# Performance work log

Hardware: AMD Instinct MI355X
Metric: run time of the kernel (lower is better)

## Reference

```python
import jax, jax.numpy as jnp
import numpy as np
from functools import partial

B, D, H, T = 1024, 512, 1024, 64  # batch, latent dim, MLP hidden, time points


def setup_inputs() -> dict:
    key = jax.random.key(0)
    k0, k1, k2, k3, k4 = jax.random.split(key, 5)
    z0 = jax.random.normal(k0, (B, D), dtype=jnp.float32)
    # strictly increasing time grid, modest dt for a stable tanh-MLP vector field
    t = jnp.arange(T, dtype=jnp.float32) * 0.02
    # 2-layer tanh MLP ode_func: dz/dt = tanh(z @ W1 + b1) @ W2 + b2
    W1 = jax.random.normal(k1, (D, H), dtype=jnp.float32) * (1.0 / np.sqrt(D))
    b1 = jnp.zeros((H,), dtype=jnp.float32)
    W2 = jax.random.normal(k2, (H, D), dtype=jnp.float32) * (1.0 / np.sqrt(H))
    b2 = jnp.zeros((D,), dtype=jnp.float32)
    return {"z0": z0, "t": t, "W1": W1, "b1": b1, "W2": W2, "b2": b2}


def _ode_func(z, W1, b1, W2, b2):
    # autonomous latent vector field: [B, D] -> [B, D]
    return jnp.tanh(z @ W1 + b1) @ W2 + b2


def reference(z0, t, W1, b1, W2, b2):
    """odeint(ode_func, z0, t, method='rk4'): one classical RK4 step per interval.
    Returns trajectory [T, B, D] with traj[0] == z0 (torchdiffeq convention)."""
    f = partial(_ode_func, W1=W1, b1=b1, W2=W2, b2=b2)
    dts = t[1:] - t[:-1]  # [T-1]

    def step(z, dt):
        k1 = f(z)
        k2 = f(z + 0.5 * dt * k1)
        k3 = f(z + 0.5 * dt * k2)
        k4 = f(z + dt * k3)
        z_new = z + (dt / 6.0) * (k1 + 2.0 * k2 + 2.0 * k3 + k4)
        return z_new, z_new

    _, traj = jax.lax.scan(step, z0, dts)  # [T-1, B, D]
    return jnp.concatenate([z0[None], traj], axis=0)  # [T, B, D]
```

## Files before the change

kernel.cpp:

```cpp
#include <hip/hip_runtime.h>
#include <hip/hip_bf16.h>

#define BATCH 1024
#define DLAT  512
#define HHID  1024
#define TPTS  64
#define BD    (BATCH * DLAT)

#define NBLK 256
#define NTHR 512
#define RGN  16


typedef __attribute__((ext_vector_type(8))) short short8;
typedef __attribute__((ext_vector_type(4))) float f32x4;

__device__ __forceinline__ short f2bf(float x) {
    __hip_bfloat16 h = __float2bfloat16(x);
    return __builtin_bit_cast(short, h);
}
__device__ __forceinline__ float fast_tanh(float x) {
    x = fminf(9.f, fmaxf(-9.f, x));
    const float e = __expf(2.f * x);
    return (e - 1.f) / (e + 1.f);
}

__device__ __forceinline__ void rg_barrier(int* bar, int cidx, int target, int tid)
{
    __syncthreads();
    if (tid == 0) {
        atomicAdd(&bar[cidx], 1);
        while (__hip_atomic_load(&bar[cidx], __ATOMIC_RELAXED,
                                 __HIP_MEMORY_SCOPE_AGENT) < target) {
            __builtin_amdgcn_s_sleep(2);
        }
    }
    __syncthreads();
    asm volatile("buffer_inv\n\ts_waitcnt vmcnt(0)" ::: "memory");
}

__global__ __launch_bounds__(NTHR) void ode_coop(
    const float* __restrict__ z0, const float* __restrict__ t,
    const float* __restrict__ W1, const float* __restrict__ b1,
    const float* __restrict__ W2, const float* __restrict__ b2,
    short* __restrict__ zf, short* __restrict__ Hf,
    int* __restrict__ bar, int* __restrict__ xcnt,
    float* __restrict__ traj)
{
    __shared__ __align__(16) short W1L[4 * 16 * 64 * 8];
    __shared__ __align__(16) short W2L[2 * 32 * 64 * 8];
    __shared__ float b1L[64];
    __shared__ float b2L[32];
    __shared__ int slotS;

    const int tid  = threadIdx.x;
    const int lane = tid & 63;
    const int w    = tid >> 6;
    const int q    = lane >> 4;
    const int cl   = lane & 15;

    unsigned int xcc;
    asm("s_getreg_b32 %0, hwreg(HW_REG_XCC_ID)" : "=s"(xcc));
    xcc &= 7u;
    if (tid == 0) slotS = atomicAdd(&xcnt[xcc], 1);
    __syncthreads();
    const int slot = slotS & 31;
    const int rg   = (int)xcc * 2 + (slot >> 4);
    const int cg   = slot & 15;
    const int cidx = rg * 32;

    for (int i = tid; i < 4 * 16 * 64; i += NTHR) {
        const int ct = i >> 10, kt = (i >> 6) & 15, l = i & 63;
        const int k0 = kt * 32 + (l >> 4) * 8;
        const int n  = cg * 64 + ct * 16 + (l & 15);
        short8 v;
#pragma unroll
        for (int j = 0; j < 8; ++j) v[j] = f2bf(W1[(size_t)(k0 + j) * HHID + n]);
        *(short8*)&W1L[i * 8] = v;
    }
    for (int i = tid; i < 2 * 32 * 64; i += NTHR) {
        const int ct = i >> 11, kt = (i >> 6) & 31, l = i & 63;
        const int k0 = kt * 32 + (l >> 4) * 8;
        const int n  = cg * 32 + ct * 16 + (l & 15);
        short8 v;
#pragma unroll
        for (int j = 0; j < 8; ++j) v[j] = f2bf(W2[(size_t)(k0 + j) * DLAT + n]);
        *(short8*)&W2L[i * 8] = v;
    }
    if (tid < 64)      b1L[tid]      = b1[cg * 64 + tid];
    else if (tid < 96) b2L[tid - 64] = b2[cg * 32 + (tid - 64)];

    const int rt   = w >> 1;
    const int c0   = (w & 1) * 2;
    const int ct2b = w & 1;
    const int rowb = rg * 64 + rt * 16 + q * 4;
    const int nb   = cg * 32 + ct2b * 16 + cl;
    const int clb  = ct2b * 16 + cl;

    const size_t zbase = ((size_t)(rg * 4 + rt) * 16 + cg) * 512 +
                         (size_t)(((clb >> 3) * 16 + q * 4) * 8 + (clb & 7));
    size_t hbase[2];
#pragma unroll
    for (int c = 0; c < 2; ++c) {
        const int colc = (c0 + c) * 16 + cl;
        hbase[c] = ((size_t)(rg * 4 + rt) * 32 + cg * 2 + (colc >> 5)) * 512 +
                   (size_t)((((colc & 31) >> 3) * 16 + q * 4) * 8 + (colc & 7));
    }

    float zreg[4], kacc[4];
#pragma unroll
    for (int reg = 0; reg < 4; ++reg) {
        const float zv = z0[(size_t)(rowb + reg) * DLAT + nb];
        zreg[reg] = zv;
        traj[(size_t)(rowb + reg) * DLAT + nb] = zv;
        zf[zbase + reg * 8] = f2bf(zv);
    }

    int target = 0;
    target += RGN; rg_barrier(bar, cidx, target, tid);

    const short* zrow = zf + (size_t)(rg * 4 + rt) * 8192  + lane * 8;
    const short* hrow = Hf + (size_t)(rg * 4 + rt) * 16384 + lane * 8;
    const short* w1p  = &W1L[c0 * 8192 + lane * 8];
    const short* w2p  = &W2L[ct2b * 16384 + lane * 8];

    for (int step = 0; step < TPTS - 1; ++step) {
        const float dt = t[step + 1] - t[step];

        if (step > 0) {
#pragma unroll
            for (int reg = 0; reg < 4; ++reg)
                traj[(size_t)step * BD + (size_t)(rowb + reg) * DLAT + nb] =
                    zreg[reg];
        }

#pragma unroll
        for (int stage = 0; stage < 4; ++stage) {
            {
                f32x4 acc0 = {0.f, 0.f, 0.f, 0.f};
                f32x4 acc1 = {0.f, 0.f, 0.f, 0.f};
#pragma unroll
                for (int kt = 0; kt < 16; ++kt) {
                    const short8 a  = *(const short8*)(zrow + kt * 512);
                    const short8 bA = *(const short8*)(w1p + kt * 512);
                    const short8 bB = *(const short8*)(w1p + 8192 + kt * 512);
                    acc0 = __builtin_amdgcn_mfma_f32_16x16x32_bf16(a, bA, acc0, 0, 0, 0);
                    acc1 = __builtin_amdgcn_mfma_f32_16x16x32_bf16(a, bB, acc1, 0, 0, 0);
                }
#pragma unroll
                for (int c = 0; c < 2; ++c) {
                    const int   cloc = (c0 + c) * 16 + cl;
                    const float bb   = b1L[cloc];
                    const f32x4 av   = c ? acc1 : acc0;
#pragma unroll
                    for (int reg = 0; reg < 4; ++reg)
                        Hf[hbase[c] + reg * 8] = f2bf(fast_tanh(av[reg] + bb));
                }
            }
            target += RGN; rg_barrier(bar, cidx, target, tid);

            {
                f32x4 acce = {0.f, 0.f, 0.f, 0.f};
                f32x4 acco = {0.f, 0.f, 0.f, 0.f};
#pragma unroll
                for (int kt = 0; kt < 32; kt += 2) {
                    const short8 a0  = *(const short8*)(hrow + kt * 512);
                    const short8 a1  = *(const short8*)(hrow + kt * 512 + 512);
                    const short8 bb0 = *(const short8*)(w2p + kt * 512);
                    const short8 bb1 = *(const short8*)(w2p + kt * 512 + 512);
                    acce = __builtin_amdgcn_mfma_f32_16x16x32_bf16(a0, bb0, acce, 0, 0, 0);
                    acco = __builtin_amdgcn_mfma_f32_16x16x32_bf16(a1, bb1, acco, 0, 0, 0);
                }
                const float bb = b2L[clb];
#pragma unroll
                for (int reg = 0; reg < 4; ++reg) {
                    const float kv = acce[reg] + acco[reg] + bb;
                    float znext;
                    if (stage == 0) {
                        kacc[reg] = kv;        znext = zreg[reg] + 0.5f * dt * kv;
                    } else if (stage == 1) {
                        kacc[reg] += 2.f * kv; znext = zreg[reg] + 0.5f * dt * kv;
                    } else if (stage == 2) {
                        kacc[reg] += 2.f * kv; znext = zreg[reg] + dt * kv;
                    } else {
                        zreg[reg] += (dt * (1.f / 6.f)) * (kacc[reg] + kv);
                        znext = zreg[reg];
                    }
                    zf[zbase + reg * 8] = f2bf(znext);
                }
            }
            target += RGN; rg_barrier(bar, cidx, target, tid);
        }
    }

#pragma unroll
    for (int reg = 0; reg < 4; ++reg)
        traj[(size_t)(TPTS - 1) * BD + (size_t)(rowb + reg) * DLAT + nb] =
            zreg[reg];
}

extern "C" void kernel_launch(void* const* d_in, const int* in_sizes, int n_in,
                              void* d_out, int out_size, void* d_ws, size_t ws_size,
                              hipStream_t stream)
{
    (void)in_sizes; (void)n_in; (void)out_size; (void)ws_size;

    const float* z0 = (const float*)d_in[0];
    const float* t  = (const float*)d_in[1];
    const float* W1 = (const float*)d_in[2];
    const float* b1 = (const float*)d_in[3];
    const float* W2 = (const float*)d_in[4];
    const float* b2 = (const float*)d_in[5];
    float*       traj = (float*)d_out;

    short* zf   = (short*)d_ws;
    short* Hf   = (short*)((char*)d_ws + (1u << 20));
    int*   bar  = (int*)((char*)d_ws + (3u << 20));
    int*   xcnt = (int*)((char*)d_ws + (3u << 20) + 2048);

    hipMemsetAsync(bar, 0, 16 * 32 * sizeof(int) + 8 * sizeof(int), stream);

    void* args[] = {&z0, &t, &W1, &b1, &W2, &b2, &zf, &Hf, &bar, &xcnt, &traj};
    hipLaunchCooperativeKernel((const void*)ode_coop, dim3(NBLK), dim3(NTHR),
                               args, 0, stream);
}
```

Before: 1.394 ms.

## Switch to 32x32x16 MFMA tiles with split-K across waves and LDS reduction

Replaces the 16x16x32 MFMA tiling with 32x32x16 MFMA tiles. Each wave now computes a partial sum over a slice of K, and the partials are combined through an LDS reduction buffer with a block-level sync. The global layouts of the bf16 z and H scratch buffers and of the LDS weight tiles are reorganised to match the new fragment shape. The aim is fewer, larger MFMA instructions and fewer operand loads per wave, at the cost of an extra __syncthreads, LDS traffic for the reduction, and higher register pressure from 16-wide accumulators.

```diff
diff --git a/kernel.cpp b/kernel.cpp
--- a/kernel.cpp
+++ b/kernel.cpp
@@ -12,8 +12,8 @@
 #define RGN  16
 
 
-typedef __attribute__((ext_vector_type(8))) short short8;
-typedef __attribute__((ext_vector_type(4))) float f32x4;
+typedef __attribute__((ext_vector_type(8)))  short short8;
+typedef __attribute__((ext_vector_type(16))) float f32x16;
 
 __device__ __forceinline__ short f2bf(float x) {
     __hip_bfloat16 h = __float2bfloat16(x);
@@ -47,8 +47,9 @@
     int* __restrict__ bar, int* __restrict__ xcnt,
     float* __restrict__ traj)
 {
-    __shared__ __align__(16) short W1L[4 * 16 * 64 * 8];
-    __shared__ __align__(16) short W2L[2 * 32 * 64 * 8];
+    __shared__ __align__(16) short W1L[32 * 2 * 64 * 8];
+    __shared__ __align__(16) short W2L[64 * 64 * 8];
+    __shared__ float Rbuf[6144];
     __shared__ float b1L[64];
     __shared__ float b2L[32];
     __shared__ int slotS;
@@ -56,8 +57,6 @@
     const int tid  = threadIdx.x;
     const int lane = tid & 63;
     const int w    = tid >> 6;
-    const int q    = lane >> 4;
-    const int cl   = lane & 15;
 
     unsigned int xcc;
     asm("s_getreg_b32 %0, hwreg(HW_REG_XCC_ID)" : "=s"(xcc));
@@ -69,19 +68,19 @@
     const int cg   = slot & 15;
     const int cidx = rg * 32;
 
-    for (int i = tid; i < 4 * 16 * 64; i += NTHR) {
-        const int ct = i >> 10, kt = (i >> 6) & 15, l = i & 63;
-        const int k0 = kt * 32 + (l >> 4) * 8;
-        const int n  = cg * 64 + ct * 16 + (l & 15);
+    for (int i = tid; i < 32 * 2 * 64; i += NTHR) {
+        const int kt = i >> 7, ct = (i >> 6) & 1, l = i & 63;
+        const int k0 = kt * 16 + (l >> 5) * 8;
+        const int n  = cg * 64 + ct * 32 + (l & 31);
         short8 v;
 #pragma unroll
         for (int j = 0; j < 8; ++j) v[j] = f2bf(W1[(size_t)(k0 + j) * HHID + n]);
         *(short8*)&W1L[i * 8] = v;
     }
-    for (int i = tid; i < 2 * 32 * 64; i += NTHR) {
-        const int ct = i >> 11, kt = (i >> 6) & 31, l = i & 63;
-        const int k0 = kt * 32 + (l >> 4) * 8;
-        const int n  = cg * 32 + ct * 16 + (l & 15);
+    for (int i = tid; i < 64 * 64; i += NTHR) {
+        const int kt = i >> 6, l = i & 63;
+        const int k0 = kt * 16 + (l >> 5) * 8;
+        const int n  = cg * 32 + (l & 31);
         short8 v;
 #pragma unroll
         for (int j = 0; j < 8; ++j) v[j] = f2bf(W2[(size_t)(k0 + j) * DLAT + n]);
@@ -90,103 +89,132 @@
     if (tid < 64)      b1L[tid]      = b1[cg * 64 + tid];
     else if (tid < 96) b2L[tid - 64] = b2[cg * 32 + (tid - 64)];
 
-    const int rt   = w >> 1;
-    const int c0   = (w & 1) * 2;
-    const int ct2b = w & 1;
-    const int rowb = rg * 64 + rt * 16 + q * 4;
-    const int nb   = cg * 32 + ct2b * 16 + cl;
-    const int clb  = ct2b * 16 + cl;
-
-    const size_t zbase = ((size_t)(rg * 4 + rt) * 16 + cg) * 512 +
-                         (size_t)(((clb >> 3) * 16 + q * 4) * 8 + (clb & 7));
-    size_t hbase[2];
-#pragma unroll
-    for (int c = 0; c < 2; ++c) {
-        const int colc = (c0 + c) * 16 + cl;
-        hbase[c] = ((size_t)(rg * 4 + rt) * 32 + cg * 2 + (colc >> 5)) * 512 +
-                   (size_t)((((colc & 31) >> 3) * 16 + q * 4) * 8 + (colc & 7));
-    }
-
+    const int tileA = w >> 1, khalf = w & 1;
+    const int rtA = tileA >> 1, ctA = tileA & 1;
+    const int tileB = w >> 2, kq = w & 3;
+    const int col32 = lane & 31;
+    const int hl4   = (lane >> 5) * 4;
+
+    const int hcl = ctA * 32 + col32;
+    const size_t hAbase = ((size_t)(rg * 2 + rtA) * 64 + cg * 4 + (hcl >> 4)) * 512
+                        + (size_t)(((hcl >> 3) & 1) * 256 + (hcl & 7));
+    const size_t zBbase = ((size_t)(rg * 2 + tileB) * 32 + cg * 2 + (col32 >> 4)) * 512
+                        + (size_t)(((col32 >> 3) & 1) * 256 + (col32 & 7));
+    const int nbcol = cg * 32 + col32;
+    const int rown0 = rg * 64 + tileB * 32 + kq * 8 + hl4;
+
+    for (int e = tid; e < 64 * 32; e += NTHR) {
+        const int row64 = e >> 5, c32 = e & 31;
+        const float v = z0[(size_t)(rg * 64 + row64) * DLAT + cg * 32 + c32];
+        traj[(size_t)(rg * 64 + row64) * DLAT + cg * 32 + c32] = v;
+        zf[((size_t)(rg * 2 + (row64 >> 5)) * 32 + cg * 2 + (c32 >> 4)) * 512 +
+           ((c32 >> 3) & 1) * 256 + (row64 & 31) * 8 + (c32 & 7)] = f2bf(v);
+    }
     float zreg[4], kacc[4];
 #pragma unroll
-    for (int reg = 0; reg < 4; ++reg) {
-        const float zv = z0[(size_t)(rowb + reg) * DLAT + nb];
-        zreg[reg] = zv;
-        traj[(size_t)(rowb + reg) * DLAT + nb] = zv;
-        zf[zbase + reg * 8] = f2bf(zv);
-    }
+    for (int i = 0; i < 4; ++i)
+        zreg[i] = z0[(size_t)(rown0 + i) * DLAT + nbcol];
 
     int target = 0;
     target += RGN; rg_barrier(bar, cidx, target, tid);
 
-    const short* zrow = zf + (size_t)(rg * 4 + rt) * 8192  + lane * 8;
-    const short* hrow = Hf + (size_t)(rg * 4 + rt) * 16384 + lane * 8;
-    const short* w1p  = &W1L[c0 * 8192 + lane * 8];
-    const short* w2p  = &W2L[ct2b * 16384 + lane * 8];
+    const short* zA  = zf + ((size_t)(rg * 2 + rtA) * 32 + khalf * 16) * 512 + lane * 8;
+    const short* hB  = Hf + ((size_t)(rg * 2 + tileB) * 64 + kq * 16) * 512 + lane * 8;
+    const short* w1p = &W1L[((khalf * 16) * 2 + ctA) * 512 + lane * 8];
+    const short* w2p = &W2L[(kq * 16) * 512 + lane * 8];
 
     for (int step = 0; step < TPTS - 1; ++step) {
         const float dt = t[step + 1] - t[step];
 
         if (step > 0) {
 #pragma unroll
-            for (int reg = 0; reg < 4; ++reg)
-                traj[(size_t)step * BD + (size_t)(rowb + reg) * DLAT + nb] =
-                    zreg[reg];
+            for (int i = 0; i < 4; ++i)
+                traj[(size_t)step * BD + (size_t)(rown0 + i) * DLAT + nbcol] =
+                    zreg[i];
         }
 
 #pragma unroll
         for (int stage = 0; stage < 4; ++stage) {
             {
-                f32x4 acc0 = {0.f, 0.f, 0.f, 0.f};
-                f32x4 acc1 = {0.f, 0.f, 0.f, 0.f};
+                f32x16 acc = {0.f,0.f,0.f,0.f, 0.f,0.f,0.f,0.f,
+                              0.f,0.f,0.f,0.f, 0.f,0.f,0.f,0.f};
 #pragma unroll
                 for (int kt = 0; kt < 16; ++kt) {
-                    const short8 a  = *(const short8*)(zrow + kt * 512);
-                    const short8 bA = *(const short8*)(w1p + kt * 512);
-                    const short8 bB = *(const short8*)(w1p + 8192 + kt * 512);
-                    acc0 = __builtin_amdgcn_mfma_f32_16x16x32_bf16(a, bA, acc0, 0, 0, 0);
-                    acc1 = __builtin_amdgcn_mfma_f32_16x16x32_bf16(a, bB, acc1, 0, 0, 0);
-                }
-#pragma unroll
-                for (int c = 0; c < 2; ++c) {
-                    const int   cloc = (c0 + c) * 16 + cl;
-                    const float bb   = b1L[cloc];
-                    const f32x4 av   = c ? acc1 : acc0;
-#pragma unroll
-                    for (int reg = 0; reg < 4; ++reg)
-                        Hf[hbase[c] + reg * 8] = f2bf(fast_tanh(av[reg] + bb));
+                    const short8 a = *(const short8*)(zA  + kt * 512);
+                    const short8 b = *(const short8*)(w1p + kt * 1024);
+                    acc = __builtin_amdgcn_mfma_f32_32x32x16_bf16(a, b, acc, 0, 0, 0);
+                }
+#pragma unroll
+                for (int h = 0; h < 2; ++h) if (khalf == h) {
+#pragma unroll
+                    for (int i = 0; i < 8; ++i) {
+                        const int r = (1 - h) * 8 + i;
+                        Rbuf[(tileA * 16 + r) * 64 + lane] = acc[r];
+                    }
+                }
+                __syncthreads();
+#pragma unroll
+                for (int h = 0; h < 2; ++h) if (khalf == h) {
+#pragma unroll
+                    for (int i = 0; i < 8; ++i) {
+                        const int r     = h * 8 + i;
+                        const int row32 = (i & 3) + 8 * (h * 2 + (i >> 2)) + hl4;
+                        const float v = acc[r] + Rbuf[(tileA * 16 + r) * 64 + lane]
+                                      + b1L[hcl];
+                        Hf[hAbase + row32 * 8] = f2bf(fast_tanh(v));
+                    }
                 }
             }
             target += RGN; rg_barrier(bar, cidx, target, tid);
 
             {
-                f32x4 acce = {0.f, 0.f, 0.f, 0.f};
-                f32x4 acco = {0.f, 0.f, 0.f, 0.f};
-#pragma unroll
-                for (int kt = 0; kt < 32; kt += 2) {
-                    const short8 a0  = *(const short8*)(hrow + kt * 512);
-                    const short8 a1  = *(const short8*)(hrow + kt * 512 + 512);
-                    const short8 bb0 = *(const short8*)(w2p + kt * 512);
-                    const short8 bb1 = *(const short8*)(w2p + kt * 512 + 512);
-                    acce = __builtin_amdgcn_mfma_f32_16x16x32_bf16(a0, bb0, acce, 0, 0, 0);
-                    acco = __builtin_amdgcn_mfma_f32_16x16x32_bf16(a1, bb1, acco, 0, 0, 0);
-                }
-                const float bb = b2L[clb];
-#pragma unroll
-                for (int reg = 0; reg < 4; ++reg) {
-                    const float kv = acce[reg] + acco[reg] + bb;
+                f32x16 acc = {0.f,0.f,0.f,0.f, 0.f,0.f,0.f,0.f,
+                              0.f,0.f,0.f,0.f, 0.f,0.f,0.f,0.f};
+#pragma unroll
+                for (int kt = 0; kt < 16; ++kt) {
+                    const short8 a = *(const short8*)(hB  + kt * 512);
+                    const short8 b = *(const short8*)(w2p + kt * 512);
+                    acc = __builtin_amdgcn_mfma_f32_32x32x16_bf16(a, b, acc, 0, 0, 0);
+                }
+#pragma unroll
+                for (int g = 0; g < 4; ++g) if (kq == g) {
+#pragma unroll
+                    for (int r = 0; r < 16; ++r) {
+                        const int og = r >> 2;
+                        if (og != g) {
+                            const int s = (g < og) ? g : g - 1;
+                            Rbuf[((tileB * 16 + r) * 3 + s) * 64 + lane] = acc[r];
+                        }
+                    }
+                }
+                __syncthreads();
+                float kvp[4];
+#pragma unroll
+                for (int g = 0; g < 4; ++g) if (kq == g) {
+#pragma unroll
+                    for (int i = 0; i < 4; ++i) {
+                        const int r = g * 4 + i;
+                        kvp[i] = acc[r]
+                               + Rbuf[((tileB * 16 + r) * 3 + 0) * 64 + lane]
+                               + Rbuf[((tileB * 16 + r) * 3 + 1) * 64 + lane]
+                               + Rbuf[((tileB * 16 + r) * 3 + 2) * 64 + lane];
+                    }
+                }
+#pragma unroll
+                for (int i = 0; i < 4; ++i) {
+                    const float kv = kvp[i] + b2L[col32];
                     float znext;
                     if (stage == 0) {
-                        kacc[reg] = kv;        znext = zreg[reg] + 0.5f * dt * kv;
+                        kacc[i] = kv;        znext = zreg[i] + 0.5f * dt * kv;
                     } else if (stage == 1) {
-                        kacc[reg] += 2.f * kv; znext = zreg[reg] + 0.5f * dt * kv;
+                        kacc[i] += 2.f * kv; znext = zreg[i] + 0.5f * dt * kv;
                     } else if (stage == 2) {
-                        kacc[reg] += 2.f * kv; znext = zreg[reg] + dt * kv;
+                        kacc[i] += 2.f * kv; znext = zreg[i] + dt * kv;
                     } else {
-                        zreg[reg] += (dt * (1.f / 6.f)) * (kacc[reg] + kv);
-                        znext = zreg[reg];
-                    }
-                    zf[zbase + reg * 8] = f2bf(znext);
+                        zreg[i] += (dt * (1.f / 6.f)) * (kacc[i] + kv);
+                        znext = zreg[i];
+                    }
+                    zf[zBbase + (size_t)(kq * 8 + hl4 + i) * 8] = f2bf(znext);
                 }
             }
             target += RGN; rg_barrier(bar, cidx, target, tid);
@@ -194,9 +222,9 @@
     }
 
 #pragma unroll
-    for (int reg = 0; reg < 4; ++reg)
-        traj[(size_t)(TPTS - 1) * BD + (size_t)(rowb + reg) * DLAT + nb] =
-            zreg[reg];
+    for (int i = 0; i < 4; ++i)
+        traj[(size_t)(TPTS - 1) * BD + (size_t)(rown0 + i) * DLAT + nbcol] =
+            zreg[i];
 }
 
 extern "C" void kernel_launch(void* const* d_in, const int* in_sizes, int n_in,
```

Result: no change. 1.389 ms (-0.3%).

## Replace counter barriers with per-block flags and double-buffer z state

Applied to the files above, without the earlier changes.

Swaps the shared atomic-counter barrier for per-block progress flags. Each block bumps its own z or H flag, and its waves poll the 16 peer flags in its row group with a wave-wide all-check. The z bf16 buffer is now double-buffered, so a block can write the next z while peers may still be reading the previous one. This is meant to cut atomic contention on one counter and relax the full barrier into point-to-point dependencies. In exchange it adds more polling traffic and relies on the flag ordering being exactly right for correctness.

```diff
diff --git a/kernel.cpp b/kernel.cpp
--- a/kernel.cpp
+++ b/kernel.cpp
@@ -25,17 +25,13 @@
     return (e - 1.f) / (e + 1.f);
 }
 
-__device__ __forceinline__ void rg_barrier(int* bar, int cidx, int target, int tid)
-{
-    __syncthreads();
-    if (tid == 0) {
-        atomicAdd(&bar[cidx], 1);
-        while (__hip_atomic_load(&bar[cidx], __ATOMIC_RELAXED,
-                                 __HIP_MEMORY_SCOPE_AGENT) < target) {
-            __builtin_amdgcn_s_sleep(2);
-        }
-    }
-    __syncthreads();
+__device__ __forceinline__ void wait_flags(const int* fp, int need) {
+    while (true) {
+        const int v = __hip_atomic_load(fp, __ATOMIC_RELAXED,
+                                        __HIP_MEMORY_SCOPE_AGENT);
+        if (__all(v >= need)) break;
+        __builtin_amdgcn_s_sleep(2);
+    }
     asm volatile("buffer_inv\n\ts_waitcnt vmcnt(0)" ::: "memory");
 }
 
@@ -44,8 +40,8 @@
     const float* __restrict__ W1, const float* __restrict__ b1,
     const float* __restrict__ W2, const float* __restrict__ b2,
     short* __restrict__ zf, short* __restrict__ Hf,
-    int* __restrict__ bar, int* __restrict__ xcnt,
-    float* __restrict__ traj)
+    int* __restrict__ zfl, int* __restrict__ hfl,
+    int* __restrict__ xcnt, float* __restrict__ traj)
 {
     __shared__ __align__(16) short W1L[4 * 16 * 64 * 8];
     __shared__ __align__(16) short W2L[2 * 32 * 64 * 8];
@@ -67,7 +63,13 @@
     const int slot = slotS & 31;
     const int rg   = (int)xcc * 2 + (slot >> 4);
     const int cg   = slot & 15;
-    const int cidx = rg * 32;
+
+    int* zflg = zfl + rg * 64;
+    int* hflg = hfl + rg * 64;
+    int* zown = zflg + cg * 4;
+    int* hown = hflg + cg * 4;
+    const int* zpoll = zflg + (lane & 15) * 4;
+    const int* hpoll = hflg + (lane & 15) * 4;
 
     for (int i = tid; i < 4 * 16 * 64; i += NTHR) {
         const int ct = i >> 10, kt = (i >> 6) & 15, l = i & 63;
@@ -107,23 +109,26 @@
                    (size_t)((((colc & 31) >> 3) * 16 + q * 4) * 8 + (colc & 7));
     }
 
+    short* zf0 = zf;
+    short* zf1 = zf + 524288;
+
     float zreg[4], kacc[4];
 #pragma unroll
     for (int reg = 0; reg < 4; ++reg) {
         const float zv = z0[(size_t)(rowb + reg) * DLAT + nb];
         zreg[reg] = zv;
         traj[(size_t)(rowb + reg) * DLAT + nb] = zv;
-        zf[zbase + reg * 8] = f2bf(zv);
-    }
-
-    int target = 0;
-    target += RGN; rg_barrier(bar, cidx, target, tid);
-
-    const short* zrow = zf + (size_t)(rg * 4 + rt) * 8192  + lane * 8;
+        zf1[zbase + reg * 8] = f2bf(zv);
+    }
+    __syncthreads();
+    if (tid == 0) atomicAdd(zown, 1);
+
+    const size_t zrowoff = (size_t)(rg * 4 + rt) * 8192 + lane * 8;
     const short* hrow = Hf + (size_t)(rg * 4 + rt) * 16384 + lane * 8;
     const short* w1p  = &W1L[c0 * 8192 + lane * 8];
     const short* w2p  = &W2L[ct2b * 16384 + lane * 8];
 
+    int g = 1;
     for (int step = 0; step < TPTS - 1; ++step) {
         const float dt = t[step + 1] - t[step];
 
@@ -136,7 +141,9 @@
 
 #pragma unroll
         for (int stage = 0; stage < 4; ++stage) {
+            wait_flags(zpoll, g);
             {
+                const short* zrow = ((g & 1) ? zf1 : zf0) + zrowoff;
                 f32x4 acc0 = {0.f, 0.f, 0.f, 0.f};
                 f32x4 acc1 = {0.f, 0.f, 0.f, 0.f};
 #pragma unroll
@@ -157,8 +164,10 @@
                         Hf[hbase[c] + reg * 8] = f2bf(fast_tanh(av[reg] + bb));
                 }
             }
-            target += RGN; rg_barrier(bar, cidx, target, tid);
-
+            __syncthreads();
+            if (tid == 0) atomicAdd(hown, 1);
+
+            wait_flags(hpoll, g);
             {
                 f32x4 acce = {0.f, 0.f, 0.f, 0.f};
                 f32x4 acco = {0.f, 0.f, 0.f, 0.f};
@@ -172,6 +181,7 @@
                     acco = __builtin_amdgcn_mfma_f32_16x16x32_bf16(a1, bb1, acco, 0, 0, 0);
                 }
                 const float bb = b2L[clb];
+                short* zw = (((g + 1) & 1) ? zf1 : zf0);
 #pragma unroll
                 for (int reg = 0; reg < 4; ++reg) {
                     const float kv = acce[reg] + acco[reg] + bb;
@@ -186,10 +196,12 @@
                         zreg[reg] += (dt * (1.f / 6.f)) * (kacc[reg] + kv);
                         znext = zreg[reg];
                     }
-                    zf[zbase + reg * 8] = f2bf(znext);
+                    zw[zbase + reg * 8] = f2bf(znext);
                 }
             }
-            target += RGN; rg_barrier(bar, cidx, target, tid);
+            __syncthreads();
+            if (tid == 0) atomicAdd(zown, 1);
+            ++g;
         }
     }
 
@@ -214,13 +226,14 @@
     float*       traj = (float*)d_out;
 
     short* zf   = (short*)d_ws;
-    short* Hf   = (short*)((char*)d_ws + (1u << 20));
-    int*   bar  = (int*)((char*)d_ws + (3u << 20));
-    int*   xcnt = (int*)((char*)d_ws + (3u << 20) + 2048);
-
-    hipMemsetAsync(bar, 0, 16 * 32 * sizeof(int) + 8 * sizeof(int), stream);
-
-    void* args[] = {&z0, &t, &W1, &b1, &W2, &b2, &zf, &Hf, &bar, &xcnt, &traj};
+    short* Hf   = (short*)((char*)d_ws + (2u << 20));
+    int*   zfl  = (int*)((char*)d_ws + (4u << 20));
+    int*   hfl  = (int*)((char*)d_ws + (4u << 20) + 4096);
+    int*   xcnt = (int*)((char*)d_ws + (4u << 20) + 8192);
+
+    hipMemsetAsync(zfl, 0, 8192 + 32, stream);
+
+    void* args[] = {&z0, &t, &W1, &b1, &W2, &b2, &zf, &Hf, &zfl, &hfl, &xcnt, &traj};
     hipLaunchCooperativeKernel((const void*)ode_coop, dim3(NBLK), dim3(NTHR),
                                args, 0, stream);
 }
```

Result: slower. 3.775 ms (+170.9%).
